# Kernel optimization log

Hardware: AMD Instinct MI355X
Metric: run time of the kernel (lower is better)

Reference implementation:

```python
import jax, jax.numpy as jnp
import numpy as np

GROUP_SIZE = 64

def _dequant(wq, scale, zero):
    # HQQ groupwise dequant: W = (Wq - zero) * scale, groups along input dim.
    out_dim, in_dim = wq.shape
    g = in_dim // GROUP_SIZE
    w = (wq.astype(jnp.float32).reshape(out_dim, g, GROUP_SIZE) - zero[:, :, None]) * scale[:, :, None]
    return w.reshape(out_dim, in_dim)

def setup_inputs() -> dict:
    key = jax.random.key(0)
    ks = jax.random.split(key, 10)
    T, H, I = 256, 4096, 14336
    G1, G2 = H // GROUP_SIZE, I // GROUP_SIZE  # 64, 224
    x = jax.random.normal(ks[0], (T, H), dtype=jnp.float32)
    w1_q = jax.random.randint(ks[1], (I, H), 0, 16, dtype=jnp.int32)
    w1_scale = jax.random.uniform(ks[2], (I, G1), dtype=jnp.float32) * 0.02
    w1_zero = jax.random.uniform(ks[3], (I, G1), dtype=jnp.float32) * 8.0
    w3_q = jax.random.randint(ks[4], (I, H), 0, 16, dtype=jnp.int32)
    w3_scale = jax.random.uniform(ks[5], (I, G1), dtype=jnp.float32) * 0.02
    w3_zero = jax.random.uniform(ks[6], (I, G1), dtype=jnp.float32) * 8.0
    w2_q = jax.random.randint(ks[7], (H, I), 0, 16, dtype=jnp.int32)
    w2_scale = jax.random.uniform(ks[8], (H, G2), dtype=jnp.float32) * 0.02
    w2_zero = jax.random.uniform(ks[9], (H, G2), dtype=jnp.float32) * 8.0
    return {"x": x, "w1_q": w1_q, "w1_scale": w1_scale, "w1_zero": w1_zero,
            "w3_q": w3_q, "w3_scale": w3_scale, "w3_zero": w3_zero,
            "w2_q": w2_q, "w2_scale": w2_scale, "w2_zero": w2_zero}

def reference(x, w1_q, w1_scale, w1_zero, w3_q, w3_scale, w3_zero, w2_q, w2_scale, w2_zero):
    w1 = _dequant(w1_q, w1_scale, w1_zero)  # [I, H]
    w3 = _dequant(w3_q, w3_scale, w3_zero)  # [I, H]
    w2 = _dequant(w2_q, w2_scale, w2_zero)  # [H, I]
    gate = jax.nn.silu(jnp.einsum('th,ih->ti', x, w1))  # [T, I]
    up = jnp.einsum('th,ih->ti', x, w3)                 # [T, I]
    return jnp.einsum('ti,hi->th', gate * up, w2)       # [T, H]
```

## Files before the change

### kernel.cpp

```cpp
#include <hip/hip_runtime.h>
#include <cstdint>
#include <cstddef>

#define T_DIM 256
#define H_DIM 4096
#define I_DIM 14336

typedef __attribute__((ext_vector_type(8))) short s8v;
typedef __attribute__((ext_vector_type(4))) float f4v;

static constexpr size_t XS_BYTES   = (size_t)T_DIM * H_DIM * 2;
static constexpr size_t ACT_OFF    = XS_BYTES;
static constexpr size_t ACT_BYTES  = (size_t)T_DIM * I_DIM * 2;
static constexpr size_t PART_OFF   = ACT_OFF + ACT_BYTES;
static constexpr size_t PART_BYTES = 8ull * T_DIM * H_DIM * 4;
static constexpr size_t WS_NEEDED  = PART_OFF + PART_BYTES;

__device__ __forceinline__ unsigned short f2bf(float f) {
    unsigned u = __builtin_bit_cast(unsigned, f);
    u += 0x7fffu + ((u >> 16) & 1u);
    return (unsigned short)(u >> 16);
}

__device__ __forceinline__ void g2lds16(const void* g, void* l) {
    __builtin_amdgcn_global_load_lds(
        (const __attribute__((address_space(1))) unsigned int*)g,
        (__attribute__((address_space(3))) unsigned int*)l,
        16, 0, 0);
}

__device__ __forceinline__ s8v dq8(const int4 qa, const int4 qb, float s, float ns) {
    union { unsigned short u[8]; s8v v; } r;
    r.u[0] = f2bf(fmaf((float)qa.x, s, ns));
    r.u[1] = f2bf(fmaf((float)qa.y, s, ns));
    r.u[2] = f2bf(fmaf((float)qa.z, s, ns));
    r.u[3] = f2bf(fmaf((float)qa.w, s, ns));
    r.u[4] = f2bf(fmaf((float)qb.x, s, ns));
    r.u[5] = f2bf(fmaf((float)qb.y, s, ns));
    r.u[6] = f2bf(fmaf((float)qb.z, s, ns));
    r.u[7] = f2bf(fmaf((float)qb.w, s, ns));
    return r.v;
}

__global__ __launch_bounds__(256) void k_prep(const float* __restrict__ x,
                                              unsigned short* __restrict__ xs) {
    int gs   = blockIdx.x * 256 + threadIdx.x;
    int kt   = gs >> 11;
    int rem  = gs & 2047;
    int row  = rem >> 3;
    int slot = rem & 7;
    const float* xp = x + (size_t)row * H_DIM + kt * 64 + slot * 8;
    float4 a = *(const float4*)xp;
    float4 b = *(const float4*)(xp + 4);
    union { unsigned short u[8]; s8v v; } r;
    r.u[0] = f2bf(a.x); r.u[1] = f2bf(a.y); r.u[2] = f2bf(a.z); r.u[3] = f2bf(a.w);
    r.u[4] = f2bf(b.x); r.u[5] = f2bf(b.y); r.u[6] = f2bf(b.z); r.u[7] = f2bf(b.w);
    size_t di = (size_t)kt * 16384 + (size_t)row * 64 + (size_t)((slot ^ (row & 7)) * 8);
    *(s8v*)(xs + di) = r.v;
}

__global__ __launch_bounds__(512, 2) void k_gemm1(
    const int* __restrict__ w1q, const float* __restrict__ w1s, const float* __restrict__ w1z,
    const int* __restrict__ w3q, const float* __restrict__ w3s, const float* __restrict__ w3z,
    const unsigned short* __restrict__ xs, unsigned short* __restrict__ act)
{
    __shared__ unsigned char lds[49152];
    const int tid  = threadIdx.x;
    const int blk  = blockIdx.x;
    const int n0   = blk * 64;
    const int wid  = tid >> 6;
    const int lane = tid & 63;
    const int wr   = wid >> 1;
    const int wc   = wid & 1;
    const int lr   = lane & 15;
    const int lkb  = lane >> 4;
    const int aswz = (lr & 7) << 4;

    const int srow  = tid >> 3;
    const int sslot = tid & 7;
    const size_t grow = (size_t)(n0 + srow) * H_DIM + (size_t)sslot * 8;
    const int wbyte = srow * 128 + ((sslot * 16) ^ ((srow & 7) << 4));
    const float* s1p = w1s + (size_t)(n0 + srow) * 64;
    const float* z1p = w1z + (size_t)(n0 + srow) * 64;
    const float* s3p = w3s + (size_t)(n0 + srow) * 64;
    const float* z3p = w3z + (size_t)(n0 + srow) * 64;

    f4v accg[4][2], accu[4][2];
    const f4v fz = {0.f, 0.f, 0.f, 0.f};
    #pragma unroll
    for (int i = 0; i < 4; ++i)
        #pragma unroll
        for (int j = 0; j < 2; ++j) { accg[i][j] = fz; accu[i][j] = fz; }

    const unsigned char* xsb = (const unsigned char*)xs;

    for (int kt = 0; kt < 64; ++kt) {
        {
            const unsigned char* gsrc = xsb + (size_t)kt * 32768 + (size_t)wid * 1024
                                            + (size_t)lane * 16;
            unsigned char* ldst = lds + wid * 1024;
            #pragma unroll
            for (int j = 0; j < 4; ++j)
                g2lds16(gsrc + j * 8192, ldst + j * 8192);
        }
        {
            const int4* p1 = (const int4*)(w1q + grow + (size_t)kt * 64);
            const int4* p3 = (const int4*)(w3q + grow + (size_t)kt * 64);
            int4 q1a = p1[0], q1b = p1[1];
            int4 q3a = p3[0], q3b = p3[1];
            float s1 = s1p[kt]; float ns1 = -z1p[kt] * s1;
            float s3 = s3p[kt]; float ns3 = -z3p[kt] * s3;
            *(s8v*)(lds + 32768 + wbyte) = dq8(q1a, q1b, s1, ns1);
            *(s8v*)(lds + 40960 + wbyte) = dq8(q3a, q3b, s3, ns3);
        }
        __syncthreads();
        #pragma unroll
        for (int kf = 0; kf < 2; ++kf) {
            const int kb = (kf * 64 + lkb * 16) ^ aswz;
            s8v a[4];
            #pragma unroll
            for (int mf = 0; mf < 4; ++mf)
                a[mf] = *(const s8v*)(lds + (wr * 64 + mf * 16 + lr) * 128 + kb);
            s8v b1[2], b3[2];
            #pragma unroll
            for (int nf = 0; nf < 2; ++nf) {
                const int rbo = (wc * 32 + nf * 16 + lr) * 128 + kb;
                b1[nf] = *(const s8v*)(lds + 32768 + rbo);
                b3[nf] = *(const s8v*)(lds + 40960 + rbo);
            }
            #pragma unroll
            for (int mf = 0; mf < 4; ++mf)
                #pragma unroll
                for (int nf = 0; nf < 2; ++nf) {
                    accg[mf][nf] = __builtin_amdgcn_mfma_f32_16x16x32_bf16(a[mf], b1[nf], accg[mf][nf], 0, 0, 0);
                    accu[mf][nf] = __builtin_amdgcn_mfma_f32_16x16x32_bf16(a[mf], b3[nf], accu[mf][nf], 0, 0, 0);
                }
        }
        __syncthreads();
    }

    unsigned char* actb = (unsigned char*)act + (size_t)blk * 32768;
    #pragma unroll
    for (int mf = 0; mf < 4; ++mf)
        #pragma unroll
        for (int nf = 0; nf < 2; ++nf)
            #pragma unroll
            for (int r = 0; r < 4; ++r) {
                const int m  = wr * 64 + mf * 16 + lkb * 4 + r;
                const int nl = wc * 32 + nf * 16 + lr;
                float g = accg[mf][nf][r];
                float u = accu[mf][nf][r];
                float sg = g / (1.0f + __expf(-g));
                *(unsigned short*)(actb + ((m * 128 + nl * 2) ^ ((m & 7) << 4))) = f2bf(sg * u);
            }
}

template<bool ATOMIC>
__global__ __launch_bounds__(512, 2) void k_gemm2(
    const int* __restrict__ w2q, const float* __restrict__ w2s, const float* __restrict__ w2z,
    const unsigned short* __restrict__ act, float* __restrict__ outp)
{
    __shared__ unsigned char lds[49152];
    const int tid  = threadIdx.x;
    const int nb   = blockIdx.x & 31;
    const int kc   = blockIdx.x >> 5;
    const int n0   = nb * 128;
    const int wid  = tid >> 6;
    const int lane = tid & 63;
    const int wr   = wid >> 2;
    const int wc   = wid & 3;
    const int lr   = lane & 15;
    const int lkb  = lane >> 4;
    const int aswz = (lr & 7) << 4;

    const int srow = tid >> 2;
    const int ss2  = (tid & 3) * 2;
    const size_t grow = (size_t)(n0 + srow) * I_DIM + (size_t)ss2 * 8;
    const int wb0 = srow * 128 + ((ss2 * 16)       ^ ((srow & 7) << 4));
    const int wb1 = srow * 128 + (((ss2 + 1) * 16) ^ ((srow & 7) << 4));
    const float* s2p = w2s + (size_t)(n0 + srow) * 224;
    const float* z2p = w2z + (size_t)(n0 + srow) * 224;

    f4v acc[8][2];
    const f4v fz = {0.f, 0.f, 0.f, 0.f};
    #pragma unroll
    for (int i = 0; i < 8; ++i) { acc[i][0] = fz; acc[i][1] = fz; }

    const unsigned char* actb = (const unsigned char*)act;
    const int kt0 = kc * 28;

    for (int kk = 0; kk < 28; ++kk) {
        const int kt = kt0 + kk;
        {
            const unsigned char* gsrc = actb + (size_t)kt * 32768 + (size_t)wid * 1024
                                             + (size_t)lane * 16;
            unsigned char* ldst = lds + wid * 1024;
            #pragma unroll
            for (int j = 0; j < 4; ++j)
                g2lds16(gsrc + j * 8192, ldst + j * 8192);
        }
        {
            const int4* p2 = (const int4*)(w2q + grow + (size_t)kt * 64);
            int4 qa = p2[0], qb = p2[1], qc = p2[2], qd = p2[3];
            float s2 = s2p[kt]; float ns2 = -z2p[kt] * s2;
            *(s8v*)(lds + 32768 + wb0) = dq8(qa, qb, s2, ns2);
            *(s8v*)(lds + 32768 + wb1) = dq8(qc, qd, s2, ns2);
        }
        __syncthreads();
        #pragma unroll
        for (int kf = 0; kf < 2; ++kf) {
            const int kb = (kf * 64 + lkb * 16) ^ aswz;
            s8v b2[2];
            #pragma unroll
            for (int nf = 0; nf < 2; ++nf)
                b2[nf] = *(const s8v*)(lds + 32768 + (wc * 32 + nf * 16 + lr) * 128 + kb);
            #pragma unroll
            for (int mf = 0; mf < 8; ++mf) {
                s8v a = *(const s8v*)(lds + (wr * 128 + mf * 16 + lr) * 128 + kb);
                acc[mf][0] = __builtin_amdgcn_mfma_f32_16x16x32_bf16(a, b2[0], acc[mf][0], 0, 0, 0);
                acc[mf][1] = __builtin_amdgcn_mfma_f32_16x16x32_bf16(a, b2[1], acc[mf][1], 0, 0, 0);
            }
        }
        __syncthreads();
    }

    float* pout = outp + (ATOMIC ? 0 : (size_t)kc * ((size_t)T_DIM * H_DIM));
    #pragma unroll
    for (int mf = 0; mf < 8; ++mf)
        #pragma unroll
        for (int nf = 0; nf < 2; ++nf)
            #pragma unroll
            for (int r = 0; r < 4; ++r) {
                const int m = wr * 128 + mf * 16 + lkb * 4 + r;
                const int n = n0 + wc * 32 + nf * 16 + lr;
                if (ATOMIC) atomicAdd(&outp[(size_t)m * H_DIM + n], acc[mf][nf][r]);
                else        pout[(size_t)m * H_DIM + n] = acc[mf][nf][r];
            }
}

__global__ __launch_bounds__(256) void k_reduce(const f4v* __restrict__ p,
                                                f4v* __restrict__ o) {
    int i = blockIdx.x * 256 + threadIdx.x;
    f4v s = p[i];
    #pragma unroll
    for (int c = 1; c < 8; ++c) s += p[(size_t)c * 262144 + i];
    o[i] = s;
}

__global__ __launch_bounds__(256) void k_zero(f4v* __restrict__ o) {
    o[blockIdx.x * 256 + threadIdx.x] = (f4v){0.f, 0.f, 0.f, 0.f};
}

extern "C" void kernel_launch(void* const* d_in, const int* in_sizes, int n_in,
                              void* d_out, int out_size, void* d_ws, size_t ws_size,
                              hipStream_t stream) {
    const float* x   = (const float*)d_in[0];
    const int*   w1q = (const int*)  d_in[1];
    const float* w1s = (const float*)d_in[2];
    const float* w1z = (const float*)d_in[3];
    const int*   w3q = (const int*)  d_in[4];
    const float* w3s = (const float*)d_in[5];
    const float* w3z = (const float*)d_in[6];
    const int*   w2q = (const int*)  d_in[7];
    const float* w2s = (const float*)d_in[8];
    const float* w2z = (const float*)d_in[9];
    float* outp = (float*)d_out;

    unsigned short* xs  = (unsigned short*)d_ws;
    unsigned short* act = (unsigned short*)((char*)d_ws + ACT_OFF);
    float*          prt = (float*)((char*)d_ws + PART_OFF);
    const bool partials = (ws_size >= WS_NEEDED);

    k_prep<<<512, 256, 0, stream>>>(x, xs);
    k_gemm1<<<224, 512, 0, stream>>>(w1q, w1s, w1z, w3q, w3s, w3z, xs, act);
    if (partials) {
        k_gemm2<false><<<256, 512, 0, stream>>>(w2q, w2s, w2z, act, prt);
        k_reduce<<<1024, 256, 0, stream>>>((const f4v*)prt, (f4v*)outp);
    } else {
        k_zero<<<1024, 256, 0, stream>>>((f4v*)outp);
        k_gemm2<true><<<256, 512, 0, stream>>>(w2q, w2s, w2z, act, outp);
    }
}
```

Measured before the change: 284.9 us.

## Software-pipeline both GEMMs with register prefetch and double-buffered LDS

Both dequant GEMM kernels stop using direct global-to-LDS loads and instead prefetch the next K-tile's activation and quantized weight data into registers while the current tile is multiplied out of a second LDS buffer. The bank-conflict swizzle moves from the global layout of the bf16 intermediates into the LDS store, so the prep kernel and the activation writer now emit plain row-major tiles. This is meant to hide global memory latency behind MFMA work. In exchange, per-block LDS doubles to 96KB, which can prevent two 512-thread blocks from sharing a CU. Holding two prefetch structs in registers also raises register pressure under the 512-thread launch bounds and may cause spills.

```diff
diff --git a/kernel.cpp b/kernel.cpp
--- a/kernel.cpp
+++ b/kernel.cpp
@@ -20,13 +20,6 @@
     unsigned u = __builtin_bit_cast(unsigned, f);
     u += 0x7fffu + ((u >> 16) & 1u);
     return (unsigned short)(u >> 16);
-}
-
-__device__ __forceinline__ void g2lds16(const void* g, void* l) {
-    __builtin_amdgcn_global_load_lds(
-        (const __attribute__((address_space(1))) unsigned int*)g,
-        (__attribute__((address_space(3))) unsigned int*)l,
-        16, 0, 0);
 }
 
 __device__ __forceinline__ s8v dq8(const int4 qa, const int4 qb, float s, float ns) {
@@ -55,16 +48,17 @@
     union { unsigned short u[8]; s8v v; } r;
     r.u[0] = f2bf(a.x); r.u[1] = f2bf(a.y); r.u[2] = f2bf(a.z); r.u[3] = f2bf(a.w);
     r.u[4] = f2bf(b.x); r.u[5] = f2bf(b.y); r.u[6] = f2bf(b.z); r.u[7] = f2bf(b.w);
-    size_t di = (size_t)kt * 16384 + (size_t)row * 64 + (size_t)((slot ^ (row & 7)) * 8);
-    *(s8v*)(xs + di) = r.v;
-}
+    *(s8v*)(xs + (size_t)kt * 16384 + (size_t)row * 64 + (size_t)slot * 8) = r.v;
+}
+
+struct P1 { int4 x0, x1, x2, x3, q1a, q1b, q3a, q3b; float s1, z1, s3, z3; };
 
 __global__ __launch_bounds__(512, 2) void k_gemm1(
     const int* __restrict__ w1q, const float* __restrict__ w1s, const float* __restrict__ w1z,
     const int* __restrict__ w3q, const float* __restrict__ w3s, const float* __restrict__ w3z,
     const unsigned short* __restrict__ xs, unsigned short* __restrict__ act)
 {
-    __shared__ unsigned char lds[49152];
+    __shared__ unsigned char lds[2][49152];
     const int tid  = threadIdx.x;
     const int blk  = blockIdx.x;
     const int n0   = blk * 64;
@@ -76,14 +70,14 @@
     const int lkb  = lane >> 4;
     const int aswz = (lr & 7) << 4;
 
-    const int srow  = tid >> 3;
-    const int sslot = tid & 7;
-    const size_t grow = (size_t)(n0 + srow) * H_DIM + (size_t)sslot * 8;
-    const int wbyte = srow * 128 + ((sslot * 16) ^ ((srow & 7) << 4));
-    const float* s1p = w1s + (size_t)(n0 + srow) * 64;
-    const float* z1p = w1z + (size_t)(n0 + srow) * 64;
-    const float* s3p = w3s + (size_t)(n0 + srow) * 64;
-    const float* z3p = w3z + (size_t)(n0 + srow) * 64;
+    const int sr = tid >> 3, sl = tid & 7;
+    const int sbyte = sr * 128 + ((sl * 16) ^ ((sr & 7) << 4));
+    const int4*  xbase = (const int4*)xs;
+    const size_t wrow  = (size_t)(n0 + sr) * H_DIM;
+    const float* s1p = w1s + (size_t)(n0 + sr) * 64;
+    const float* z1p = w1z + (size_t)(n0 + sr) * 64;
+    const float* s3p = w3s + (size_t)(n0 + sr) * 64;
+    const float* z3p = w3z + (size_t)(n0 + sr) * 64;
 
     f4v accg[4][2], accu[4][2];
     const f4v fz = {0.f, 0.f, 0.f, 0.f};
@@ -92,41 +86,36 @@
         #pragma unroll
         for (int j = 0; j < 2; ++j) { accg[i][j] = fz; accu[i][j] = fz; }
 
-    const unsigned char* xsb = (const unsigned char*)xs;
-
-    for (int kt = 0; kt < 64; ++kt) {
-        {
-            const unsigned char* gsrc = xsb + (size_t)kt * 32768 + (size_t)wid * 1024
-                                            + (size_t)lane * 16;
-            unsigned char* ldst = lds + wid * 1024;
-            #pragma unroll
-            for (int j = 0; j < 4; ++j)
-                g2lds16(gsrc + j * 8192, ldst + j * 8192);
-        }
-        {
-            const int4* p1 = (const int4*)(w1q + grow + (size_t)kt * 64);
-            const int4* p3 = (const int4*)(w3q + grow + (size_t)kt * 64);
-            int4 q1a = p1[0], q1b = p1[1];
-            int4 q3a = p3[0], q3b = p3[1];
-            float s1 = s1p[kt]; float ns1 = -z1p[kt] * s1;
-            float s3 = s3p[kt]; float ns3 = -z3p[kt] * s3;
-            *(s8v*)(lds + 32768 + wbyte) = dq8(q1a, q1b, s1, ns1);
-            *(s8v*)(lds + 40960 + wbyte) = dq8(q3a, q3b, s3, ns3);
-        }
-        __syncthreads();
+    auto load = [&](int kt, P1& p) {
+        const int4* xp = xbase + kt * 2048 + sr * 8 + sl;
+        p.x0 = xp[0]; p.x1 = xp[512]; p.x2 = xp[1024]; p.x3 = xp[1536];
+        const int4* p1 = (const int4*)(w1q + wrow + kt * 64 + sl * 8);
+        const int4* p3 = (const int4*)(w3q + wrow + kt * 64 + sl * 8);
+        p.q1a = p1[0]; p.q1b = p1[1]; p.q3a = p3[0]; p.q3b = p3[1];
+        p.s1 = s1p[kt]; p.z1 = z1p[kt]; p.s3 = s3p[kt]; p.z3 = z3p[kt];
+    };
+    auto store = [&](const P1& p, unsigned char* b) {
+        *(int4*)(b + sbyte)         = p.x0;
+        *(int4*)(b + sbyte + 8192)  = p.x1;
+        *(int4*)(b + sbyte + 16384) = p.x2;
+        *(int4*)(b + sbyte + 24576) = p.x3;
+        *(s8v*)(b + 32768 + sbyte) = dq8(p.q1a, p.q1b, p.s1, -p.z1 * p.s1);
+        *(s8v*)(b + 40960 + sbyte) = dq8(p.q3a, p.q3b, p.s3, -p.z3 * p.s3);
+    };
+    auto compute = [&](const unsigned char* b) {
         #pragma unroll
         for (int kf = 0; kf < 2; ++kf) {
             const int kb = (kf * 64 + lkb * 16) ^ aswz;
             s8v a[4];
             #pragma unroll
             for (int mf = 0; mf < 4; ++mf)
-                a[mf] = *(const s8v*)(lds + (wr * 64 + mf * 16 + lr) * 128 + kb);
+                a[mf] = *(const s8v*)(b + (wr * 64 + mf * 16 + lr) * 128 + kb);
             s8v b1[2], b3[2];
             #pragma unroll
             for (int nf = 0; nf < 2; ++nf) {
                 const int rbo = (wc * 32 + nf * 16 + lr) * 128 + kb;
-                b1[nf] = *(const s8v*)(lds + 32768 + rbo);
-                b3[nf] = *(const s8v*)(lds + 40960 + rbo);
+                b1[nf] = *(const s8v*)(b + 32768 + rbo);
+                b3[nf] = *(const s8v*)(b + 40960 + rbo);
             }
             #pragma unroll
             for (int mf = 0; mf < 4; ++mf)
@@ -136,6 +125,25 @@
                     accu[mf][nf] = __builtin_amdgcn_mfma_f32_16x16x32_bf16(a[mf], b3[nf], accu[mf][nf], 0, 0, 0);
                 }
         }
+    };
+
+    P1 A, B;
+    load(0, A);
+    store(A, lds[0]);
+    load(1, B);
+    __syncthreads();
+
+    for (int it = 0; it < 32; ++it) {
+        const int t = it * 2;
+        load(t + 2 > 63 ? 63 : t + 2, A);
+        compute(lds[0]);
+        __syncthreads();
+        store(B, lds[1]);
+        __syncthreads();
+        load(t + 3 > 63 ? 63 : t + 3, B);
+        compute(lds[1]);
+        __syncthreads();
+        store(A, lds[0]);
         __syncthreads();
     }
 
@@ -151,16 +159,18 @@
                 float g = accg[mf][nf][r];
                 float u = accu[mf][nf][r];
                 float sg = g / (1.0f + __expf(-g));
-                *(unsigned short*)(actb + ((m * 128 + nl * 2) ^ ((m & 7) << 4))) = f2bf(sg * u);
+                *(unsigned short*)(actb + m * 128 + nl * 2) = f2bf(sg * u);
             }
 }
+
+struct P2 { int4 a0, a1, a2, a3, q0, q1, q2, q3; float s2, z2; };
 
 template<bool ATOMIC>
 __global__ __launch_bounds__(512, 2) void k_gemm2(
     const int* __restrict__ w2q, const float* __restrict__ w2s, const float* __restrict__ w2z,
     const unsigned short* __restrict__ act, float* __restrict__ outp)
 {
-    __shared__ unsigned char lds[49152];
+    __shared__ unsigned char lds[2][49152];
     const int tid  = threadIdx.x;
     const int nb   = blockIdx.x & 31;
     const int kc   = blockIdx.x >> 5;
@@ -173,54 +183,72 @@
     const int lkb  = lane >> 4;
     const int aswz = (lr & 7) << 4;
 
-    const int srow = tid >> 2;
-    const int ss2  = (tid & 3) * 2;
-    const size_t grow = (size_t)(n0 + srow) * I_DIM + (size_t)ss2 * 8;
-    const int wb0 = srow * 128 + ((ss2 * 16)       ^ ((srow & 7) << 4));
-    const int wb1 = srow * 128 + (((ss2 + 1) * 16) ^ ((srow & 7) << 4));
-    const float* s2p = w2s + (size_t)(n0 + srow) * 224;
-    const float* z2p = w2z + (size_t)(n0 + srow) * 224;
+    const int sr = tid >> 3, sl = tid & 7;
+    const int abyte = sr * 128 + ((sl * 16) ^ ((sr & 7) << 4));
+    const int r2 = tid >> 2, sq = tid & 3;
+    const int wb0 = r2 * 128 + (((sq * 2) * 16)     ^ ((r2 & 7) << 4));
+    const int wb1 = r2 * 128 + (((sq * 2 + 1) * 16) ^ ((r2 & 7) << 4));
+    const int4*  abase = (const int4*)act;
+    const size_t w2row = (size_t)(n0 + r2) * I_DIM;
+    const float* s2p = w2s + (size_t)(n0 + r2) * 224;
+    const float* z2p = w2z + (size_t)(n0 + r2) * 224;
 
     f4v acc[8][2];
     const f4v fz = {0.f, 0.f, 0.f, 0.f};
     #pragma unroll
     for (int i = 0; i < 8; ++i) { acc[i][0] = fz; acc[i][1] = fz; }
 
-    const unsigned char* actb = (const unsigned char*)act;
-    const int kt0 = kc * 28;
-
-    for (int kk = 0; kk < 28; ++kk) {
-        const int kt = kt0 + kk;
-        {
-            const unsigned char* gsrc = actb + (size_t)kt * 32768 + (size_t)wid * 1024
-                                             + (size_t)lane * 16;
-            unsigned char* ldst = lds + wid * 1024;
-            #pragma unroll
-            for (int j = 0; j < 4; ++j)
-                g2lds16(gsrc + j * 8192, ldst + j * 8192);
-        }
-        {
-            const int4* p2 = (const int4*)(w2q + grow + (size_t)kt * 64);
-            int4 qa = p2[0], qb = p2[1], qc = p2[2], qd = p2[3];
-            float s2 = s2p[kt]; float ns2 = -z2p[kt] * s2;
-            *(s8v*)(lds + 32768 + wb0) = dq8(qa, qb, s2, ns2);
-            *(s8v*)(lds + 32768 + wb1) = dq8(qc, qd, s2, ns2);
-        }
-        __syncthreads();
+    auto load = [&](int kt, P2& p) {
+        const int4* ap = abase + kt * 2048 + sr * 8 + sl;
+        p.a0 = ap[0]; p.a1 = ap[512]; p.a2 = ap[1024]; p.a3 = ap[1536];
+        const int4* wp = (const int4*)(w2q + w2row + kt * 64 + sq * 16);
+        p.q0 = wp[0]; p.q1 = wp[1]; p.q2 = wp[2]; p.q3 = wp[3];
+        p.s2 = s2p[kt]; p.z2 = z2p[kt];
+    };
+    auto store = [&](const P2& p, unsigned char* b) {
+        *(int4*)(b + abyte)         = p.a0;
+        *(int4*)(b + abyte + 8192)  = p.a1;
+        *(int4*)(b + abyte + 16384) = p.a2;
+        *(int4*)(b + abyte + 24576) = p.a3;
+        float ns = -p.z2 * p.s2;
+        *(s8v*)(b + 32768 + wb0) = dq8(p.q0, p.q1, p.s2, ns);
+        *(s8v*)(b + 32768 + wb1) = dq8(p.q2, p.q3, p.s2, ns);
+    };
+    auto compute = [&](const unsigned char* b) {
         #pragma unroll
         for (int kf = 0; kf < 2; ++kf) {
             const int kb = (kf * 64 + lkb * 16) ^ aswz;
-            s8v b2[2];
+            s8v bfr[2];
             #pragma unroll
             for (int nf = 0; nf < 2; ++nf)
-                b2[nf] = *(const s8v*)(lds + 32768 + (wc * 32 + nf * 16 + lr) * 128 + kb);
+                bfr[nf] = *(const s8v*)(b + 32768 + (wc * 32 + nf * 16 + lr) * 128 + kb);
             #pragma unroll
             for (int mf = 0; mf < 8; ++mf) {
-                s8v a = *(const s8v*)(lds + (wr * 128 + mf * 16 + lr) * 128 + kb);
-                acc[mf][0] = __builtin_amdgcn_mfma_f32_16x16x32_bf16(a, b2[0], acc[mf][0], 0, 0, 0);
-                acc[mf][1] = __builtin_amdgcn_mfma_f32_16x16x32_bf16(a, b2[1], acc[mf][1], 0, 0, 0);
+                s8v a = *(const s8v*)(b + (wr * 128 + mf * 16 + lr) * 128 + kb);
+                acc[mf][0] = __builtin_amdgcn_mfma_f32_16x16x32_bf16(a, bfr[0], acc[mf][0], 0, 0, 0);
+                acc[mf][1] = __builtin_amdgcn_mfma_f32_16x16x32_bf16(a, bfr[1], acc[mf][1], 0, 0, 0);
             }
         }
+    };
+
+    const int kt0 = kc * 28;
+    P2 A, B;
+    load(kt0, A);
+    store(A, lds[0]);
+    load(kt0 + 1, B);
+    __syncthreads();
+
+    for (int it = 0; it < 14; ++it) {
+        const int t = it * 2;
+        load(kt0 + (t + 2 > 27 ? 27 : t + 2), A);
+        compute(lds[0]);
+        __syncthreads();
+        store(B, lds[1]);
+        __syncthreads();
+        load(kt0 + (t + 3 > 27 ? 27 : t + 3), B);
+        compute(lds[1]);
+        __syncthreads();
+        store(A, lds[0]);
         __syncthreads();
     }
 
```

Result: slower. 296.7 us (+4.2%).
